# Optimization experiments

Measured on AMD Instinct MI355X. Metric: run time of the kernel, lower is better.

The kernel has to match this reference:

```python
import jax, jax.numpy as jnp
import numpy as np

NUM_PHRASE = 8
HDIM = 256
NUM_HEADS = 8
NUM_LAYERS = 3
MIN_DIST = 2


def sine_pos(mask, num_feats, temperature=10000.0):
    # PositionEmbeddingSine (1D, DETR-style, normalize=False)
    B, L = mask.shape
    x_embed = jnp.cumsum(mask.astype(jnp.float32), axis=1)            # [B,L]
    dim_t = jnp.arange(num_feats, dtype=jnp.float32)
    dim_t = temperature ** (2.0 * jnp.floor(dim_t / 2.0) / num_feats)
    pos = x_embed[:, :, None] / dim_t                                  # [B,L,C]
    pos = jnp.stack([jnp.sin(pos[:, :, 0::2]), jnp.cos(pos[:, :, 1::2])], axis=3)
    return pos.reshape(B, L, num_feats)


def layer_norm(x, g, b, eps=1e-5):
    mu = jnp.mean(x, axis=-1, keepdims=True)
    var = jnp.mean((x - mu) ** 2, axis=-1, keepdims=True)
    return (x - mu) / jnp.sqrt(var + eps) * g + b


def mha(q, k, v, key_mask, in_w, in_b, out_w, out_b, nheads):
    # torch nn.MultiheadAttention (batch_first, eval/no-dropout), averaged attn weights
    B, Lq, C = q.shape
    Dh = C // nheads
    qp = (q @ in_w[:, :C] + in_b[:C]).reshape(B, Lq, nheads, Dh)
    kp = (k @ in_w[:, C:2 * C] + in_b[C:2 * C]).reshape(B, -1, nheads, Dh)
    vp = (v @ in_w[:, 2 * C:] + in_b[2 * C:]).reshape(B, -1, nheads, Dh)
    scores = jnp.einsum('bqhd,bkhd->bhqk', qp, kp) / jnp.sqrt(jnp.float32(Dh))
    scores = jnp.where(key_mask[:, None, None, :], scores, -jnp.inf)
    attn = jax.nn.softmax(scores, axis=-1)
    out = jnp.einsum('bhqk,bkhd->bqhd', attn, vp).reshape(B, Lq, C)
    return out @ out_w + out_b, jnp.mean(attn, axis=1)


def cross_attention(x, y, mask, qw, qb, kvw, kvb, inw, inb, ow, ob, g0, b0, lw, lb, g1, b1):
    C = x.shape[-1]
    q = x @ qw + qb
    kv = y @ kvw + kvb
    k, v = kv[..., :C], kv[..., C:]
    q_att, attn = mha(q, k, v, mask, inw, inb, ow, ob, NUM_HEADS)
    x = layer_norm(x + q_att, g0, b0)
    update = jax.nn.relu(x @ lw + lb)
    x = layer_norm(x + update, g1, b1)
    return x, attn


def _select_one(entropy_b, mask_b):
    # greedy highest-entropy selection with min-distance suppression (1D NMS)
    P, MD = NUM_PHRASE, MIN_DIST
    score = jnp.where(mask_b, entropy_b, -jnp.inf)
    order = jnp.argsort(-score).astype(jnp.int32)   # valid indices first, descending entropy

    def step(carry, idx):
        sel, cnt = carry
        dists = jnp.where(sel >= 0, jnp.abs(idx - sel), 1000000)
        ok = mask_b[idx] & (cnt < P) & (jnp.min(dists) >= MD)
        new_sel = jnp.where(ok, sel.at[jnp.minimum(cnt, P - 1)].set(idx), sel)
        return (new_sel, cnt + ok.astype(jnp.int32)), None

    init = (jnp.full((P,), -1, jnp.int32), jnp.int32(0))
    (sel, cnt), _ = jax.lax.scan(step, init, order)
    last = sel[jnp.maximum(cnt - 1, 0)]
    return jnp.where(jnp.arange(P) < cnt, sel, last)   # pad by repeating last


def phrase_generate(txt_emb, txt_mask, video_feats, video_mask,
                    word_proj_w, word_proj_b, video_proj_w, video_proj_b,
                    q_w, q_b, kv_w, kv_b, in_w, in_b, out_w, out_b,
                    ln0_g, ln0_b, lin_w, lin_b, ln1_g, ln1_b, eos_slot):
    B, L, C = txt_emb.shape
    word_emb = txt_emb[:, 1:]
    word_mask = txt_mask[:, 1:]
    word_pe = word_emb + sine_pos(word_mask, C)

    # word importance via video cross-attention entropy
    wp = word_pe @ word_proj_w + word_proj_b                      # [B,Lw,C]
    vp = video_feats @ video_proj_w + video_proj_b                # [B,T,C]
    sim = jnp.einsum('blc,btc->blt', wp, vp)                      # [B,Lw,T]
    sim = jnp.where(video_mask[:, None, :], sim, -jnp.inf)
    attn_weights = jax.nn.softmax(sim, axis=2)
    entropy = -jnp.sum(attn_weights * jnp.log(attn_weights + 1e-6), axis=2)  # [B,Lw]

    sel = jax.vmap(_select_one)(entropy, word_mask)               # [B,P] int32
    phrase_slot = jnp.take_along_axis(word_pe, sel[:, :, None], axis=1)      # [B,P,C]

    slot_sim = None
    for i in range(NUM_LAYERS):
        phrase_slot, slot_sim = cross_attention(
            phrase_slot, word_pe, word_mask,
            q_w[i], q_b[i], kv_w[i], kv_b[i], in_w[i], in_b[i], out_w[i], out_b[i],
            ln0_g[i], ln0_b[i], lin_w[i], lin_b[i], ln1_g[i], ln1_b[i])

    eos = jnp.broadcast_to(eos_slot, (B, 1, C))
    return phrase_slot, attn_weights, slot_sim, eos


def setup_inputs() -> dict:
    key = jax.random.key(0)
    ks = jax.random.split(key, 16)
    B, L, T, C, NL = 128, 257, 1024, HDIM, NUM_LAYERS
    s = 0.02
    inp = {
        'txt_emb': jax.random.normal(ks[0], (B, L, C), jnp.float32),
        'txt_mask': jnp.ones((B, L), jnp.bool_),
        'video_feats': jax.random.normal(ks[1], (B, T, C), jnp.float32),
        'video_mask': jnp.ones((B, T), jnp.bool_),
        'word_proj_w': jax.random.normal(ks[2], (C, C)) * s,
        'word_proj_b': jnp.zeros((C,)),
        'video_proj_w': jax.random.normal(ks[3], (C, C)) * s,
        'video_proj_b': jnp.zeros((C,)),
        'q_w': jax.random.normal(ks[4], (NL, C, C)) * s,
        'q_b': jnp.zeros((NL, C)),
        'kv_w': jax.random.normal(ks[5], (NL, C, 2 * C)) * s,
        'kv_b': jnp.zeros((NL, 2 * C)),
        'in_w': jax.random.normal(ks[6], (NL, C, 3 * C)) * s,
        'in_b': jnp.zeros((NL, 3 * C)),
        'out_w': jax.random.normal(ks[7], (NL, C, C)) * s,
        'out_b': jnp.zeros((NL, C)),
        'ln0_g': jnp.ones((NL, C)),
        'ln0_b': jnp.zeros((NL, C)),
        'lin_w': jax.random.normal(ks[8], (NL, C, C)) * s,
        'lin_b': jnp.zeros((NL, C)),
        'ln1_g': jnp.ones((NL, C)),
        'ln1_b': jnp.zeros((NL, C)),
        'eos_slot': jax.random.normal(ks[9], (1, 1, C)),
    }
    return inp


def reference(txt_emb, txt_mask, video_feats, video_mask,
              word_proj_w, word_proj_b, video_proj_w, video_proj_b,
              q_w, q_b, kv_w, kv_b, in_w, in_b, out_w, out_b,
              ln0_g, ln0_b, lin_w, lin_b, ln1_g, ln1_b, eos_slot):
    return phrase_generate(txt_emb, txt_mask, video_feats, video_mask,
                           word_proj_w, word_proj_b, video_proj_w, video_proj_b,
                           q_w, q_b, kv_w, kv_b, in_w, in_b, out_w, out_b,
                           ln0_g, ln0_b, lin_w, lin_b, ln1_g, ln1_b, eos_slot)
```

## Files before the change

### kernel.cpp

```cpp
#include <hip/hip_runtime.h>
#include <math.h>

#define BB 128
#define LFULL 257
#define LW 256
#define TT 1024
#define CC 256
#define NH 8
#define DHD 32
#define PP 8
#define NLAY 3

typedef __bf16 bf16x8 __attribute__((ext_vector_type(8)));
typedef __bf16 bf16x4 __attribute__((ext_vector_type(4)));
typedef float  f32x4  __attribute__((ext_vector_type(4)));

__device__ __forceinline__ float blockReduceSum(float v, volatile float* lds) {
#pragma unroll
    for (int m = 32; m >= 1; m >>= 1) v += __shfl_xor(v, m);
    __syncthreads();
    if ((threadIdx.x & 63) == 0) lds[threadIdx.x >> 6] = v;
    __syncthreads();
    return lds[0] + lds[1] + lds[2] + lds[3];
}
__device__ __forceinline__ float blockReduceMax(float v, volatile float* lds) {
#pragma unroll
    for (int m = 32; m >= 1; m >>= 1) v = fmaxf(v, __shfl_xor(v, m));
    __syncthreads();
    if ((threadIdx.x & 63) == 0) lds[threadIdx.x >> 6] = v;
    __syncthreads();
    return fmaxf(fmaxf(lds[0], lds[1]), fmaxf(lds[2], lds[3]));
}


__device__ __forceinline__ int ldsoff(int row, int col) {
    return ((row >> 6) << 11)
         + ((((row >> 4) & 3) << 2) + (col >> 3)) * 128
         + ((row & 15) << 3) + (col & 7);
}

template<int SPLIT, int B_F32, int OUT_SPLIT>
__global__ __launch_bounds__(512, 4) void gemm_mfma(
    const __bf16* __restrict__ Ahi, const __bf16* __restrict__ Alo, int lda, long long sA,
    const void* __restrict__ Bhp, const void* __restrict__ Blp, int ldb, long long sB,
    const float* __restrict__ bias,
    float* __restrict__ Cf, __bf16* __restrict__ Chi, __bf16* __restrict__ Clo,
    int ldc, long long sC, int M, int N, int K)
{
    __shared__ __bf16 sAh[4096];
    __shared__ __bf16 sAl[SPLIT ? 4096 : 1];
    __shared__ __bf16 sBh[4096];
    __shared__ __bf16 sBl[SPLIT ? 4096 : 1];

    const int tid = threadIdx.x;
    const int n0 = blockIdx.x * 128;
    const int m0 = blockIdx.y * 128;
    const long long bz = blockIdx.z;
    const __bf16* Ah = Ahi + bz * sA;
    const __bf16* Al = SPLIT ? (Alo + bz * sA) : nullptr;

    const int wv = tid >> 6, lane = tid & 63;
    const int wm = (wv & 1) << 6;
    const int wn = (wv >> 1) << 5;
    const int lr = lane & 15, quad = lane >> 4;

    const int sr = tid >> 2;
    const int sc = (tid & 3) << 3;

    const int abase = ((wm >> 6) << 11) + (lane << 3);
    const int bbase = ((wn >> 6) << 11) + (((wn >> 4) & 3) << 9) + (lane << 3);

    f32x4 acc[4][2];
#pragma unroll
    for (int i = 0; i < 4; ++i)
#pragma unroll
        for (int j = 0; j < 2; ++j) acc[i][j] = (f32x4)(0.f);

    for (int k0 = 0; k0 < K; k0 += 32) {
        {
            int off = ldsoff(sr, sc);
            *(bf16x8*)&sAh[off] =
                *(const bf16x8*)&Ah[(long long)(m0 + sr) * lda + k0 + sc];
            if constexpr (SPLIT)
                *(bf16x8*)&sAl[off] =
                    *(const bf16x8*)&Al[(long long)(m0 + sr) * lda + k0 + sc];
        }
        if constexpr (B_F32) {
            const float* Bf = (const float*)Bhp + bz * sB;
            const float* src = &Bf[(long long)(n0 + sr) * ldb + k0 + sc];
            float4 f0 = *(const float4*)&src[0];
            float4 f1 = *(const float4*)&src[4];
            bf16x8 h8, l8;
            h8[0] = (__bf16)f0.x; l8[0] = (__bf16)(f0.x - (float)h8[0]);
            h8[1] = (__bf16)f0.y; l8[1] = (__bf16)(f0.y - (float)h8[1]);
            h8[2] = (__bf16)f0.z; l8[2] = (__bf16)(f0.z - (float)h8[2]);
            h8[3] = (__bf16)f0.w; l8[3] = (__bf16)(f0.w - (float)h8[3]);
            h8[4] = (__bf16)f1.x; l8[4] = (__bf16)(f1.x - (float)h8[4]);
            h8[5] = (__bf16)f1.y; l8[5] = (__bf16)(f1.y - (float)h8[5]);
            h8[6] = (__bf16)f1.z; l8[6] = (__bf16)(f1.z - (float)h8[6]);
            h8[7] = (__bf16)f1.w; l8[7] = (__bf16)(f1.w - (float)h8[7]);
            int off = ldsoff(sr, sc);
            *(bf16x8*)&sBh[off] = h8;
            *(bf16x8*)&sBl[off] = l8;
        } else {
            const __bf16* Bh = (const __bf16*)Bhp + bz * sB;
            int off = ldsoff(sr, sc);
            *(bf16x8*)&sBh[off] =
                *(const bf16x8*)&Bh[(long long)(n0 + sr) * ldb + k0 + sc];
            if constexpr (SPLIT) {
                const __bf16* Bl = (const __bf16*)Blp + bz * sB;
                *(bf16x8*)&sBl[off] =
                    *(const bf16x8*)&Bl[(long long)(n0 + sr) * ldb + k0 + sc];
            }
        }
        __syncthreads();

        bf16x8 fah[4], fbh[2];
        bf16x8 fal[4], fbl[2];
#pragma unroll
        for (int i = 0; i < 4; ++i) {
            fah[i] = *(const bf16x8*)&sAh[abase + i * 512];
            if constexpr (SPLIT)
                fal[i] = *(const bf16x8*)&sAl[abase + i * 512];
        }
#pragma unroll
        for (int j = 0; j < 2; ++j) {
            fbh[j] = *(const bf16x8*)&sBh[bbase + j * 512];
            if constexpr (SPLIT)
                fbl[j] = *(const bf16x8*)&sBl[bbase + j * 512];
        }
#pragma unroll
        for (int i = 0; i < 4; ++i)
#pragma unroll
            for (int j = 0; j < 2; ++j) {
                if constexpr (SPLIT) {
                    acc[i][j] = __builtin_amdgcn_mfma_f32_16x16x32_bf16(fal[i], fbh[j], acc[i][j], 0, 0, 0);
                    acc[i][j] = __builtin_amdgcn_mfma_f32_16x16x32_bf16(fah[i], fbl[j], acc[i][j], 0, 0, 0);
                }
                acc[i][j] = __builtin_amdgcn_mfma_f32_16x16x32_bf16(fah[i], fbh[j], acc[i][j], 0, 0, 0);
            }
        __syncthreads();
    }

#pragma unroll
    for (int i = 0; i < 4; ++i)
#pragma unroll
        for (int j = 0; j < 2; ++j) {
            int col = n0 + wn + j * 16 + lr;
            int row0 = m0 + wm + i * 16 + quad * 4;
            float bv = bias ? bias[col] : 0.f;
#pragma unroll
            for (int r = 0; r < 4; ++r) {
                float v = acc[i][j][r] + bv;
                long long off = (long long)(row0 + r) * ldc + col + bz * sC;
                if constexpr (OUT_SPLIT) {
                    __bf16 h = (__bf16)v;
                    Chi[off] = h;
                    Clo[off] = (__bf16)(v - (float)h);
                } else {
                    Cf[off] = v;
                }
            }
        }
}

#define GTS 64
#define GKT 16
#define GPAD 68

template<int TRANSB, int RELU, int TRANSC>
__global__ __launch_bounds__(256) void gemm_f32(
    const float* __restrict__ A, int lda, long long sA,
    const float* __restrict__ Bm, int ldb, long long sB,
    const float* __restrict__ bias,
    float* __restrict__ C, int ldc, long long sC,
    int M, int N, int K)
{
    __shared__ float As[GKT][GPAD];
    __shared__ float Bs[GKT][GPAD];
    const int tid = threadIdx.x;
    const int tx = tid & 15, ty = tid >> 4;
    const int n0 = blockIdx.x * GTS;
    const int m0 = blockIdx.y * GTS;
    const long long bz = blockIdx.z;
    const float* Ab = A + bz * sA;
    const float* Bb = Bm + bz * sB;
    float* Cb = C + bz * sC;

    const int lr = tid >> 2;
    const int lc = (tid & 3) << 2;
    const int br = tid >> 4;
    const int bc = (tid & 15) << 2;

    float acc[4][4] = {};

    for (int k0 = 0; k0 < K; k0 += GKT) {
        float4 a = *(const float4*)&Ab[(long long)(m0 + lr) * lda + k0 + lc];
        As[lc + 0][lr] = a.x; As[lc + 1][lr] = a.y;
        As[lc + 2][lr] = a.z; As[lc + 3][lr] = a.w;
        if (TRANSB) {
            float4 b = *(const float4*)&Bb[(long long)(n0 + lr) * ldb + k0 + lc];
            Bs[lc + 0][lr] = b.x; Bs[lc + 1][lr] = b.y;
            Bs[lc + 2][lr] = b.z; Bs[lc + 3][lr] = b.w;
        } else {
            float4 b = *(const float4*)&Bb[(long long)(k0 + br) * ldb + n0 + bc];
            *(float4*)&Bs[br][bc] = b;
        }
        __syncthreads();
#pragma unroll
        for (int k = 0; k < GKT; ++k) {
            float4 av = *(const float4*)&As[k][ty << 2];
            float4 bv = *(const float4*)&Bs[k][tx << 2];
            float ar[4] = {av.x, av.y, av.z, av.w};
            float brr[4] = {bv.x, bv.y, bv.z, bv.w};
#pragma unroll
            for (int i = 0; i < 4; ++i)
#pragma unroll
                for (int j = 0; j < 4; ++j)
                    acc[i][j] = fmaf(ar[i], brr[j], acc[i][j]);
        }
        __syncthreads();
    }

    float bbr[4] = {0.f, 0.f, 0.f, 0.f};
    if (bias) {
        float4 bb = *(const float4*)&bias[n0 + (tx << 2)];
        bbr[0] = bb.x; bbr[1] = bb.y; bbr[2] = bb.z; bbr[3] = bb.w;
    }
#pragma unroll
    for (int i = 0; i < 4; ++i) {
#pragma unroll
        for (int j = 0; j < 4; ++j) {
            float o = acc[i][j] + bbr[j];
            if (RELU) o = fmaxf(o, 0.f);
            if (TRANSC)
                Cb[(long long)(n0 + (tx << 2) + j) * ldc + m0 + (ty << 2) + i] = o;
            else
                Cb[(long long)(m0 + (ty << 2) + i) * ldc + n0 + (tx << 2) + j] = o;
        }
    }
}


__global__ __launch_bounds__(256) void cumsum_kernel(
    const int* __restrict__ tm, int* __restrict__ cums)
{
    int b = blockIdx.x, c = threadIdx.x;
    int lane = c & 63;
    int v = (tm[(long long)b * LFULL + 1 + c] != 0) ? 1 : 0;
#pragma unroll
    for (int off = 1; off < 64; off <<= 1) {
        int t = __shfl_up(v, off);
        if (lane >= off) v += t;
    }
    __shared__ int wsum[4];
    if (lane == 63) wsum[c >> 6] = v;
    __syncthreads();
    int w = c >> 6, add = 0;
    for (int i = 0; i < w; ++i) add += wsum[i];
    cums[b * LW + c] = v + add;
}

__global__ __launch_bounds__(256) void pe_table_kernel(float* __restrict__ petab)
{
    int n = blockIdx.x;
    int c = threadIdx.x;
    int i2 = c & ~1;
    float freq = powf(10000.0f, (float)i2 / (float)CC);
    float arg = (float)n / freq;
    petab[n * CC + c] = (c & 1) ? cosf(arg) : sinf(arg);
}

__global__ __launch_bounds__(256) void word_pe2_kernel(
    const float* __restrict__ te, const int* __restrict__ cums,
    const float* __restrict__ petab,
    __bf16* __restrict__ whi, __bf16* __restrict__ wlo)
{
    int g = blockIdx.x * 256 + threadIdx.x;
    int c0 = (g & 63) << 2;
    int l  = (g >> 6) & 255;
    int b  = g >> 14;
    int cnt = cums[b * LW + l];
    float4 s = *(const float4*)&te[((long long)(b * LFULL + 1 + l)) * CC + c0];
    float4 p = *(const float4*)&petab[cnt * CC + c0];
    float v0 = s.x + p.x, v1 = s.y + p.y, v2 = s.z + p.z, v3 = s.w + p.w;
    bf16x4 h, lo;
    h[0] = (__bf16)v0; lo[0] = (__bf16)(v0 - (float)h[0]);
    h[1] = (__bf16)v1; lo[1] = (__bf16)(v1 - (float)h[1]);
    h[2] = (__bf16)v2; lo[2] = (__bf16)(v2 - (float)h[2]);
    h[3] = (__bf16)v3; lo[3] = (__bf16)(v3 - (float)h[3]);
    long long o = ((long long)(b * LW + l)) * CC + c0;
    *(bf16x4*)&whi[o] = h;
    *(bf16x4*)&wlo[o] = lo;
}

__global__ __launch_bounds__(256) void split_transpose_kernel(
    const float* __restrict__ W, __bf16* __restrict__ hi, __bf16* __restrict__ lo)
{
    int n = blockIdx.x, k = threadIdx.x;
    float v = W[(long long)k * CC + n];
    __bf16 h = (__bf16)v;
    hi[(long long)n * CC + k] = h;
    lo[(long long)n * CC + k] = (__bf16)(v - (float)h);
}
__global__ __launch_bounds__(256) void split_plain_kernel(
    const float* __restrict__ W, __bf16* __restrict__ hi, __bf16* __restrict__ lo)
{
    int g = blockIdx.x * 256 + threadIdx.x;
    float v = W[g];
    __bf16 h = (__bf16)v;
    hi[g] = h;
    lo[g] = (__bf16)(v - (float)h);
}
__global__ __launch_bounds__(256) void cvt_bf16_kernel(
    const float* __restrict__ src, __bf16* __restrict__ dst)
{
    int g = blockIdx.x * 256 + threadIdx.x;
    dst[g] = (__bf16)src[g];
}

__global__ __launch_bounds__(256) void softmax_entropy_kernel(
    float* __restrict__ attn, const int* __restrict__ vmask,
    float* __restrict__ ent)
{
    __shared__ float lds[4];
    long long row = blockIdx.x;
    int b = blockIdx.x >> 8;
    float* p = attn + row * TT;
    const int* m = vmask + (long long)b * TT;
    int t4 = threadIdx.x * 4;
    float4 v = *(const float4*)&p[t4];
    int4 mm4 = *(const int4*)&m[t4];
    float x[4];
    x[0] = mm4.x ? v.x : -INFINITY;
    x[1] = mm4.y ? v.y : -INFINITY;
    x[2] = mm4.z ? v.z : -INFINITY;
    x[3] = mm4.w ? v.w : -INFINITY;
    float mx = fmaxf(fmaxf(x[0], x[1]), fmaxf(x[2], x[3]));
    mx = blockReduceMax(mx, lds);
    float e[4];
    float ps = 0.f;
#pragma unroll
    for (int j = 0; j < 4; ++j) { e[j] = expf(x[j] - mx); ps += e[j]; }
    float sum = blockReduceSum(ps, lds);
    float q[4];
    float ce = 0.f;
#pragma unroll
    for (int j = 0; j < 4; ++j) {
        q[j] = e[j] / sum;
        ce += q[j] * logf(q[j] + 1e-6f);
    }
    ce = blockReduceSum(ce, lds);
    *(float4*)&p[t4] = make_float4(q[0], q[1], q[2], q[3]);
    if (threadIdx.x == 0) ent[row] = -ce;
}

__global__ __launch_bounds__(256) void select_kernel(
    const float* __restrict__ ent, const int* __restrict__ tm,
    int* __restrict__ sel)
{
    int b = blockIdx.x;
    int l = threadIdx.x;
    __shared__ float sc[LW];
    __shared__ int ord[LW];
    __shared__ unsigned char mk[LW];
    mk[l] = (tm[(long long)b * LFULL + 1 + l] != 0);
    sc[l] = mk[l] ? ent[(long long)b * LW + l] : -INFINITY;
    __syncthreads();
    float mys = sc[l];
    int r = 0;
    for (int j = 0; j < LW; ++j) {
        float s = sc[j];
        r += (s > mys) || (s == mys && j < l);
    }
    ord[r] = l;
    __syncthreads();
    if (l == 0) {
        int chosen[PP];
        int cnt = 0;
        for (int t = 0; t < LW; ++t) {
            int idx = ord[t];
            if (!mk[idx]) continue;
            if (cnt >= PP) break;
            bool ok = true;
            for (int s2 = 0; s2 < cnt; ++s2) {
                int d = idx - chosen[s2];
                if (d < 0) d = -d;
                if (d < 2) ok = false;
            }
            if (ok) chosen[cnt++] = idx;
        }
        int last = (cnt > 0) ? chosen[cnt - 1] : -1;
        for (int p = 0; p < PP; ++p)
            sel[b * PP + p] = (p < cnt) ? chosen[p] : last;
    }
}

__global__ __launch_bounds__(256) void gather_kernel(
    const __bf16* __restrict__ whi, const __bf16* __restrict__ wlo,
    const int* __restrict__ sel, float* __restrict__ x0)
{
    int g = blockIdx.x * 256 + threadIdx.x;
    int b = g >> 11;
    int p = (g >> 8) & 7;
    int c = g & 255;
    int idx = sel[b * PP + p];
    if (idx < 0) idx = 0;
    long long off = ((long long)b * LW + idx) * CC + c;
    x0[g] = (float)whi[off] + (float)wlo[off];
}

__global__ __launch_bounds__(256) void eff_bias_kernel(
    const float* __restrict__ q_b, const float* __restrict__ kv_b,
    const float* __restrict__ in_w, const float* __restrict__ in_b,
    float* __restrict__ BQE_all, float* __restrict__ bkv3)
{
    int i = blockIdx.x / 3;
    int role = blockIdx.x % 3;
    int n = threadIdx.x;
    const float* inw = in_w + (long long)i * 196608;
    const float* inb = in_b + (long long)i * 768;
    const float* srcb;
    int co;
    float* dst;
    if (role == 0)      { srcb = q_b + i * 256;        co = 0;   dst = BQE_all + i * 256; }
    else if (role == 1) { srcb = kv_b + i * 512;       co = 256; dst = bkv3 + i * 512; }
    else                { srcb = kv_b + i * 512 + 256; co = 512; dst = bkv3 + i * 512 + 256; }
    float s = inb[co + n];
    for (int k = 0; k < CC; ++k)
        s = fmaf(srcb[k], inw[(long long)k * 768 + co + n], s);
    dst[n] = s;
}

__global__ __launch_bounds__(256) void attn_scores_kernel(
    const float* __restrict__ qp, const float* __restrict__ KV,
    const int* __restrict__ tm, float* __restrict__ attn)
{
    int b = blockIdx.x, h = blockIdx.y;
    int tid = threadIdx.x;
    __shared__ float qs[PP][DHD];
    __shared__ float sc[PP][LW];
    __shared__ float mxs[PP], sms[PP];
    {
        int q = tid >> 5, d = tid & 31;
        qs[q][d] = qp[((long long)(b * PP + q)) * CC + h * DHD + d];
    }
    __syncthreads();
    const float* kr = KV + ((long long)(b * LW + tid)) * 512 + h * DHD;
    float kreg[DHD];
#pragma unroll
    for (int j = 0; j < 8; ++j) {
        float4 f = *(const float4*)&kr[j * 4];
        kreg[j * 4 + 0] = f.x; kreg[j * 4 + 1] = f.y;
        kreg[j * 4 + 2] = f.z; kreg[j * 4 + 3] = f.w;
    }
    bool mk = tm[(long long)b * LFULL + 1 + tid] != 0;
#pragma unroll
    for (int q = 0; q < PP; ++q) {
        float s = 0.f;
#pragma unroll
        for (int d = 0; d < DHD; ++d) s = fmaf(qs[q][d], kreg[d], s);
        sc[q][tid] = mk ? s * 0.17677669529663687f : -INFINITY;
    }
    __syncthreads();
    {
        int q = tid >> 5, j = tid & 31;
        float m = -INFINITY;
        for (int kk = j; kk < LW; kk += 32) m = fmaxf(m, sc[q][kk]);
#pragma unroll
        for (int mm = 16; mm >= 1; mm >>= 1) m = fmaxf(m, __shfl_xor(m, mm, 32));
        float s = 0.f;
        for (int kk = j; kk < LW; kk += 32) s += expf(sc[q][kk] - m);
#pragma unroll
        for (int mm = 16; mm >= 1; mm >>= 1) s += __shfl_xor(s, mm, 32);
        if (j == 0) { mxs[q] = m; sms[q] = s; }
    }
    __syncthreads();
#pragma unroll
    for (int q = 0; q < PP; ++q) {
        float pv = expf(sc[q][tid] - mxs[q]) / sms[q];
        attn[(((long long)(b * NH + h)) * PP + q) * LW + tid] = pv;
    }
}

__global__ __launch_bounds__(256) void attn_out_kernel(
    const float* __restrict__ attn, const float* __restrict__ KV,
    float* __restrict__ aout)
{
    int b = blockIdx.x, q = blockIdx.y;
    int c = threadIdx.x, h = c >> 5;
    __shared__ float att[NH][LW];
#pragma unroll
    for (int hh = 0; hh < NH; ++hh)
        att[hh][c] = attn[(((long long)(b * NH + hh)) * PP + q) * LW + c];
    __syncthreads();
    const float* vpb = KV + ((long long)b * LW) * 512 + 256 + c;
    float acc = 0.f;
#pragma unroll 8
    for (int k = 0; k < LW; ++k)
        acc = fmaf(att[h][k], vpb[(long long)k * 512], acc);
    aout[((long long)(b * PP + q)) * CC + c] = acc;
}

__global__ __launch_bounds__(256) void slot_sim_kernel(
    const float* __restrict__ attn, float* __restrict__ outs)
{
    int b = blockIdx.x, q = blockIdx.y, k = threadIdx.x;
    float s = 0.f;
#pragma unroll
    for (int h = 0; h < NH; ++h)
        s += attn[(((long long)(b * NH + h)) * PP + q) * LW + k];
    outs[((long long)(b * PP + q)) * LW + k] = s * 0.125f;
}

__global__ __launch_bounds__(256) void ln_residual_kernel(
    const float* __restrict__ xin, const float* __restrict__ add,
    const float* __restrict__ g, const float* __restrict__ bta,
    float* __restrict__ out)
{
    __shared__ float lds[4];
    int r = blockIdx.x, c = threadIdx.x;
    long long idx = (long long)r * CC + c;
    float v = xin[idx] + add[idx];
    float s = blockReduceSum(v, lds);
    float mu = s * (1.0f / (float)CC);
    float d = v - mu;
    float var = blockReduceSum(d * d, lds) * (1.0f / (float)CC);
    out[idx] = d / sqrtf(var + 1e-5f) * g[c] + bta[c];
}

__global__ __launch_bounds__(256) void eos_kernel(
    const float* __restrict__ eos, float* __restrict__ outp)
{
    outp[(long long)blockIdx.x * CC + threadIdx.x] = eos[threadIdx.x];
}

extern "C" void kernel_launch(void* const* d_in, const int* in_sizes, int n_in,
                              void* d_out, int out_size, void* d_ws, size_t ws_size,
                              hipStream_t stream) {
    const float* txt_emb     = (const float*)d_in[0];
    const int*   txt_mask    = (const int*)d_in[1];
    const float* video_feats = (const float*)d_in[2];
    const int*   video_mask  = (const int*)d_in[3];
    const float* word_proj_w = (const float*)d_in[4];
    const float* word_proj_b = (const float*)d_in[5];
    const float* video_proj_w = (const float*)d_in[6];
    const float* q_w   = (const float*)d_in[8];
    const float* q_b   = (const float*)d_in[9];
    const float* kv_w  = (const float*)d_in[10];
    const float* kv_b  = (const float*)d_in[11];
    const float* in_w  = (const float*)d_in[12];
    const float* in_b  = (const float*)d_in[13];
    const float* out_w = (const float*)d_in[14];
    const float* out_b = (const float*)d_in[15];
    const float* ln0_g = (const float*)d_in[16];
    const float* ln0_b = (const float*)d_in[17];
    const float* lin_w = (const float*)d_in[18];
    const float* lin_b = (const float*)d_in[19];
    const float* ln1_g = (const float*)d_in[20];
    const float* ln1_b = (const float*)d_in[21];
    const float* eos_slot = (const float*)d_in[22];

    float* ws = (float*)d_ws;
    __bf16* wpe_hi = (__bf16*)(ws + 0LL);
    __bf16* wpe_lo = (__bf16*)(ws + 4194304LL);
    __bf16* wp_hi  = (__bf16*)(ws + 8388608LL);
    __bf16* wp_lo  = (__bf16*)(ws + 12582912LL);
    __bf16* U_hi   = (__bf16*)(ws + 16777216LL);
    __bf16* U_lo   = (__bf16*)(ws + 20971520LL);
    float*  KV     = ws + 8388608LL;
    float* ent     = ws + 25165824LL;
    int*   sel     = (int*)(ws + 25198592LL);
    float* x0      = ws + 25199616LL;
    float* x1      = ws + 25461760LL;
    float* xmid    = ws + 25723904LL;
    float* qp      = ws + 25986048LL;
    float* attnw   = ws + 26248192LL;
    float* aout    = ws + 28345344LL;
    float* qatt    = ws + 28607488LL;
    float* upd     = ws + 28869632LL;
    float* WQE_all = ws + 29131776LL;
    float* BQE_all = ws + 29328384LL;
    float* WT3f    = ws + 29329152LL;
    __bf16* WT3    = (__bf16*)(ws + 29722368LL);
    float* bkv3    = ws + 29918976LL;
    __bf16* WPT_hi = (__bf16*)(ws + 29920512LL);
    __bf16* WPT_lo = (__bf16*)(ws + 29953280LL);
    __bf16* VPS_hi = (__bf16*)(ws + 29986048LL);
    __bf16* VPS_lo = (__bf16*)(ws + 30018816LL);

    int*   cums  = (int*)(ws + 8388608LL);
    float* petab = ws + 8421376LL;

    float* outp     = (float*)d_out;
    float* out_ps   = outp;
    float* out_attn = outp + 262144LL;
    float* out_slot = outp + 33816576LL;
    float* out_eos  = outp + 34078720LL;

    cumsum_kernel<<<dim3(BB), dim3(256), 0, stream>>>(txt_mask, cums);
    pe_table_kernel<<<dim3(257), dim3(256), 0, stream>>>(petab);
    word_pe2_kernel<<<dim3(8192), dim3(256), 0, stream>>>(txt_emb, cums, petab, wpe_hi, wpe_lo);
    split_transpose_kernel<<<dim3(256), dim3(256), 0, stream>>>(word_proj_w, WPT_hi, WPT_lo);
    split_plain_kernel<<<dim3(256), dim3(256), 0, stream>>>(video_proj_w, VPS_hi, VPS_lo);
    gemm_mfma<1,0,1><<<dim3(2,256,1), dim3(512), 0, stream>>>(
        wpe_hi, wpe_lo, 256, 0, WPT_hi, WPT_lo, 256, 0, word_proj_b,
        nullptr, wp_hi, wp_lo, 256, 0, 32768, 256, 256);
    gemm_mfma<1,0,1><<<dim3(2,256,1), dim3(512), 0, stream>>>(
        wp_hi, wp_lo, 256, 0, VPS_hi, VPS_lo, 256, 0, nullptr,
        nullptr, U_hi, U_lo, 256, 0, 32768, 256, 256);
    gemm_mfma<1,1,0><<<dim3(8,2,BB), dim3(512), 0, stream>>>(
        U_hi, U_lo, 256, 65536LL, video_feats, nullptr, 256, 262144LL, nullptr,
        out_attn, nullptr, nullptr, 1024, 262144LL, 256, 1024, 256);
    softmax_entropy_kernel<<<dim3(32768), dim3(256), 0, stream>>>(out_attn, video_mask, ent);
    select_kernel<<<dim3(BB), dim3(256), 0, stream>>>(ent, txt_mask, sel);
    gather_kernel<<<dim3(1024), dim3(256), 0, stream>>>(wpe_hi, wpe_lo, sel, x0);

    gemm_f32<0,0,0><<<dim3(4,4,3), dim3(256), 0, stream>>>(
        q_w,256,65536LL, in_w,768,196608LL, nullptr, WQE_all,256,65536LL, 256,256,256);
    gemm_f32<0,0,1><<<dim3(4,4,3), dim3(256), 0, stream>>>(
        kv_w,512,131072LL, in_w+256,768,196608LL, nullptr, WT3f,256,131072LL, 256,256,256);
    gemm_f32<0,0,1><<<dim3(4,4,3), dim3(256), 0, stream>>>(
        kv_w+256,512,131072LL, in_w+512,768,196608LL, nullptr, WT3f+65536,256,131072LL, 256,256,256);
    eff_bias_kernel<<<dim3(9), dim3(256), 0, stream>>>(q_b, kv_b, in_w, in_b, BQE_all, bkv3);
    cvt_bf16_kernel<<<dim3(1536), dim3(256), 0, stream>>>(WT3f, (__bf16*)WT3);

    float* X = x0;
    for (int i = 0; i < NLAY; ++i) {
        const float* ow  = out_w + (long long)i * 65536;
        const float* ob  = out_b + (long long)i * 256;
        const float* g0  = ln0_g + (long long)i * 256;
        const float* b0  = ln0_b + (long long)i * 256;
        const float* lw  = lin_w + (long long)i * 65536;
        const float* lb  = lin_b + (long long)i * 256;
        const float* g1  = ln1_g + (long long)i * 256;
        const float* b1  = ln1_b + (long long)i * 256;

        gemm_mfma<0,0,0><<<dim3(4,256,1), dim3(512), 0, stream>>>(
            wpe_hi, nullptr, 256, 0, WT3 + (long long)i * 131072, nullptr, 256, 0,
            bkv3 + i * 512, KV, nullptr, nullptr, 512, 0, 32768, 512, 256);

        gemm_f32<0,0,0><<<dim3(4,16,1), dim3(256), 0, stream>>>(
            X,256,0, WQE_all + (long long)i*65536,256,0, BQE_all + i*256, qp,256,0, 1024,256,256);

        attn_scores_kernel<<<dim3(BB,NH), dim3(256), 0, stream>>>(qp, KV, txt_mask, attnw);
        attn_out_kernel<<<dim3(BB,PP), dim3(256), 0, stream>>>(attnw, KV, aout);
        if (i == NLAY - 1)
            slot_sim_kernel<<<dim3(BB,PP), dim3(256), 0, stream>>>(attnw, out_slot);

        gemm_f32<0,0,0><<<dim3(4,16,1), dim3(256), 0, stream>>>(
            aout,256,0, ow,256,0, ob, qatt,256,0, 1024,256,256);
        ln_residual_kernel<<<dim3(1024), dim3(256), 0, stream>>>(X, qatt, g0, b0, xmid);
        gemm_f32<0,1,0><<<dim3(4,16,1), dim3(256), 0, stream>>>(
            xmid,256,0, lw,256,0, lb, upd,256,0, 1024,256,256);
        float* Xout = (i == NLAY - 1) ? out_ps : ((X == x0) ? x1 : x0);
        ln_residual_kernel<<<dim3(1024), dim3(256), 0, stream>>>(xmid, upd, g1, b1, Xout);
        X = Xout;
    }
    eos_kernel<<<dim3(BB), dim3(256), 0, stream>>>(eos_slot, out_eos);
}
```

Baseline: 894.1 us.

## Double-buffer LDS tiles and prefetch next K tile into registers in MFMA GEMM

The GEMM kernel now keeps two LDS buffers per operand. It issues the global loads for the next K-tile into registers before the current tile's MFMAs run, then writes them to the alternate buffer afterwards. This overlaps global memory latency with compute and drops one __syncthreads per iteration. In exchange it doubles LDS use (up to 64KB with SPLIT) and raises register pressure, which may reduce occupancy under launch_bounds(512,4).

```diff
diff --git a/kernel.cpp b/kernel.cpp
--- a/kernel.cpp
+++ b/kernel.cpp
@@ -47,10 +47,10 @@
     float* __restrict__ Cf, __bf16* __restrict__ Chi, __bf16* __restrict__ Clo,
     int ldc, long long sC, int M, int N, int K)
 {
-    __shared__ __bf16 sAh[4096];
-    __shared__ __bf16 sAl[SPLIT ? 4096 : 1];
-    __shared__ __bf16 sBh[4096];
-    __shared__ __bf16 sBl[SPLIT ? 4096 : 1];
+    __shared__ __bf16 sAh[2][4096];
+    __shared__ __bf16 sAl[SPLIT ? 2 : 1][SPLIT ? 4096 : 1];
+    __shared__ __bf16 sBh[2][4096];
+    __shared__ __bf16 sBl[SPLIT ? 2 : 1][SPLIT ? 4096 : 1];
 
     const int tid = threadIdx.x;
     const int n0 = blockIdx.x * 128;
@@ -66,68 +66,80 @@
 
     const int sr = tid >> 2;
     const int sc = (tid & 3) << 3;
+    const int soff = ldsoff(sr, sc);
+    const long long aoff = (long long)(m0 + sr) * lda + sc;
+    const long long boff = (long long)(n0 + sr) * ldb + sc;
 
     const int abase = ((wm >> 6) << 11) + (lane << 3);
     const int bbase = ((wn >> 6) << 11) + (((wn >> 4) & 3) << 9) + (lane << 3);
 
-    f32x4 acc[4][2];
-#pragma unroll
-    for (int i = 0; i < 4; ++i)
-#pragma unroll
-        for (int j = 0; j < 2; ++j) acc[i][j] = (f32x4)(0.f);
-
-    for (int k0 = 0; k0 < K; k0 += 32) {
-        {
-            int off = ldsoff(sr, sc);
-            *(bf16x8*)&sAh[off] =
-                *(const bf16x8*)&Ah[(long long)(m0 + sr) * lda + k0 + sc];
-            if constexpr (SPLIT)
-                *(bf16x8*)&sAl[off] =
-                    *(const bf16x8*)&Al[(long long)(m0 + sr) * lda + k0 + sc];
-        }
+    bf16x8 rAh, rAl, rBh, rBl;
+    float4 rB0, rB1;
+
+    auto LOADREGS = [&](int k0) {
+        rAh = *(const bf16x8*)&Ah[aoff + k0];
+        if constexpr (SPLIT) rAl = *(const bf16x8*)&Al[aoff + k0];
         if constexpr (B_F32) {
             const float* Bf = (const float*)Bhp + bz * sB;
-            const float* src = &Bf[(long long)(n0 + sr) * ldb + k0 + sc];
-            float4 f0 = *(const float4*)&src[0];
-            float4 f1 = *(const float4*)&src[4];
-            bf16x8 h8, l8;
-            h8[0] = (__bf16)f0.x; l8[0] = (__bf16)(f0.x - (float)h8[0]);
-            h8[1] = (__bf16)f0.y; l8[1] = (__bf16)(f0.y - (float)h8[1]);
-            h8[2] = (__bf16)f0.z; l8[2] = (__bf16)(f0.z - (float)h8[2]);
-            h8[3] = (__bf16)f0.w; l8[3] = (__bf16)(f0.w - (float)h8[3]);
-            h8[4] = (__bf16)f1.x; l8[4] = (__bf16)(f1.x - (float)h8[4]);
-            h8[5] = (__bf16)f1.y; l8[5] = (__bf16)(f1.y - (float)h8[5]);
-            h8[6] = (__bf16)f1.z; l8[6] = (__bf16)(f1.z - (float)h8[6]);
-            h8[7] = (__bf16)f1.w; l8[7] = (__bf16)(f1.w - (float)h8[7]);
-            int off = ldsoff(sr, sc);
-            *(bf16x8*)&sBh[off] = h8;
-            *(bf16x8*)&sBl[off] = l8;
+            rB0 = *(const float4*)&Bf[boff + k0];
+            rB1 = *(const float4*)&Bf[boff + k0 + 4];
         } else {
             const __bf16* Bh = (const __bf16*)Bhp + bz * sB;
-            int off = ldsoff(sr, sc);
-            *(bf16x8*)&sBh[off] =
-                *(const bf16x8*)&Bh[(long long)(n0 + sr) * ldb + k0 + sc];
+            rBh = *(const bf16x8*)&Bh[boff + k0];
             if constexpr (SPLIT) {
                 const __bf16* Bl = (const __bf16*)Blp + bz * sB;
-                *(bf16x8*)&sBl[off] =
-                    *(const bf16x8*)&Bl[(long long)(n0 + sr) * ldb + k0 + sc];
+                rBl = *(const bf16x8*)&Bl[boff + k0];
             }
         }
+    };
+    auto WRITELDS = [&](int buf) {
+        *(bf16x8*)&sAh[buf][soff] = rAh;
+        if constexpr (SPLIT) *(bf16x8*)&sAl[buf][soff] = rAl;
+        if constexpr (B_F32) {
+            bf16x8 h8, l8;
+            h8[0] = (__bf16)rB0.x; l8[0] = (__bf16)(rB0.x - (float)h8[0]);
+            h8[1] = (__bf16)rB0.y; l8[1] = (__bf16)(rB0.y - (float)h8[1]);
+            h8[2] = (__bf16)rB0.z; l8[2] = (__bf16)(rB0.z - (float)h8[2]);
+            h8[3] = (__bf16)rB0.w; l8[3] = (__bf16)(rB0.w - (float)h8[3]);
+            h8[4] = (__bf16)rB1.x; l8[4] = (__bf16)(rB1.x - (float)h8[4]);
+            h8[5] = (__bf16)rB1.y; l8[5] = (__bf16)(rB1.y - (float)h8[5]);
+            h8[6] = (__bf16)rB1.z; l8[6] = (__bf16)(rB1.z - (float)h8[6]);
+            h8[7] = (__bf16)rB1.w; l8[7] = (__bf16)(rB1.w - (float)h8[7]);
+            *(bf16x8*)&sBh[buf][soff] = h8;
+            *(bf16x8*)&sBl[buf][soff] = l8;
+        } else {
+            *(bf16x8*)&sBh[buf][soff] = rBh;
+            if constexpr (SPLIT) *(bf16x8*)&sBl[buf][soff] = rBl;
+        }
+    };
+
+    f32x4 acc[4][2];
+#pragma unroll
+    for (int i = 0; i < 4; ++i)
+#pragma unroll
+        for (int j = 0; j < 2; ++j) acc[i][j] = (f32x4)(0.f);
+
+    const int nt = K >> 5;
+    LOADREGS(0);
+    WRITELDS(0);
+    int cur = 0;
+    for (int t = 0; t < nt; ++t) {
         __syncthreads();
+        if (t + 1 < nt) LOADREGS((t + 1) << 5);
 
         bf16x8 fah[4], fbh[2];
         bf16x8 fal[4], fbl[2];
 #pragma unroll
         for (int i = 0; i < 4; ++i) {
-            fah[i] = *(const bf16x8*)&sAh[abase + i * 512];
+            fah[i] = *(const bf16x8*)&sAh[cur][abase + i * 512];
             if constexpr (SPLIT)
-                fal[i] = *(const bf16x8*)&sAl[abase + i * 512];
+                fal[i] = *(const bf16x8*)&sAl[cur][abase + i * 512];
         }
 #pragma unroll
         for (int j = 0; j < 2; ++j) {
-            fbh[j] = *(const bf16x8*)&sBh[bbase + j * 512];
+            fbh[j] = *(const bf16x8*)&sBh[cur][bbase + j * 512];
             if constexpr (SPLIT)
-                fbl[j] = *(const bf16x8*)&sBl[bbase + j * 512];
+                fbl[j] = *(const bf16x8*)&sBl[cur][bbase + j * 512];
         }
 #pragma unroll
         for (int i = 0; i < 4; ++i)
@@ -139,7 +151,9 @@
                 }
                 acc[i][j] = __builtin_amdgcn_mfma_f32_16x16x32_bf16(fah[i], fbh[j], acc[i][j], 0, 0, 0);
             }
-        __syncthreads();
+
+        if (t + 1 < nt) WRITELDS(cur ^ 1);
+        cur ^= 1;
     }
 
 #pragma unroll
```

Result: no change. 890.7 us (-0.4%).
